# Kernel tuning notes

Measured on AMD Instinct MI355X. Metric: run time of the kernel, lower is better.

## Reference

```python
import jax, jax.numpy as jnp
import numpy as np

LOG_PROB_FACTOR = 0.5  # logProbFactor


def setup_inputs() -> dict:
    key = jax.random.key(0)
    ks = jax.random.split(key, 8)
    B, L, F, K = 2048, 512, 64, 2
    s = jax.random.randint(ks[0], (B, L), 0, K)
    W0 = jax.random.normal(ks[1], (K, F), jnp.float32) / np.sqrt(K).astype(np.float32)
    b0 = jnp.zeros((F,), jnp.float32)
    # fused LSTM weights, gate order (i, f, g, o); flax: dense_i no bias, dense_h has bias
    Wi = jax.random.normal(ks[2], (F, 4 * F), jnp.float32) / np.sqrt(F).astype(np.float32)
    Wh = jax.random.normal(ks[3], (F, 4 * F), jnp.float32) / np.sqrt(F).astype(np.float32)
    bh = jnp.zeros((4 * F,), jnp.float32)
    Wa = jax.random.normal(ks[4], (F, K), jnp.float32) / np.sqrt(F).astype(np.float32)
    ba = jnp.zeros((K,), jnp.float32)
    Wp = jax.random.normal(ks[5], (F, 1), jnp.float32) / np.sqrt(F).astype(np.float32)
    bp = jnp.zeros((1,), jnp.float32)
    return {"s": s, "W0": W0, "b0": b0, "Wi": Wi, "Wh": Wh, "bh": bh,
            "Wa": Wa, "ba": ba, "Wp": Wp, "bp": bp}


def _forward(s, W0, b0, Wi, Wh, bh, Wa, ba, Wp, bp):
    B, L = s.shape
    K, F = W0.shape
    # pad a leading zero token: input at step t is spin at site t-1
    s_pad = jnp.pad(s, ((0, 0), (1, 0)))                       # [B, L+1]
    x = jax.nn.one_hot(s_pad, K, dtype=W0.dtype) @ W0 + b0     # layer0: [B, L+1, F]
    xs = jnp.swapaxes(x, 0, 1)                                 # [L+1, B, F] time-major
    c0 = jnp.zeros((B, F), x.dtype)
    h0 = jnp.zeros((B, F), x.dtype)

    def step(carry, xt):
        c, h = carry
        g = xt @ Wi + h @ Wh + bh                              # [B, 4F]
        i, f, gg, o = jnp.split(g, 4, axis=-1)
        cn = jax.nn.sigmoid(f) * c + jax.nn.sigmoid(i) * jnp.tanh(gg)
        hn = jax.nn.sigmoid(o) * jnp.tanh(cn)
        return (cn, hn), hn

    _, ys = jax.lax.scan(step, (c0, h0), xs)                   # [L+1, B, F]

    logits = ys[:-1] @ Wa + ba                                 # [L, B, K]
    logp = jax.nn.log_softmax(logits, axis=-1) * LOG_PROB_FACTOR
    picked = jnp.take_along_axis(logp, s.T[..., None], axis=-1)[..., 0]  # [L, B]
    amp = picked.sum(axis=0)                                   # [B]
    phase = (ys[-1] @ Wp + bp)[..., 0]                         # [B]
    return amp + 1j * phase                                    # complex log-psi per sample


def reference(s, W0, b0, Wi, Wh, bh, Wa, ba, Wp, bp):
    return _forward(s, W0, b0, Wi, Wh, bh, Wa, ba, Wp, bp)
```

## Files before the change

kernel.cpp:

```cpp
#include <hip/hip_runtime.h>
#include <math.h>

typedef _Float16 f16x8 __attribute__((ext_vector_type(8)));
typedef float    f32x4 __attribute__((ext_vector_type(4)));
typedef _Float16 f16x2 __attribute__((ext_vector_type(2)));
typedef __fp16   fp16x2 __attribute__((ext_vector_type(2)));

#define B_TOT 2048
#define LSEQ  512
#define NS    4
#define LOG2E 1.44269504088896f
#define LN2   0.69314718055995f

#define MFMA16(A, B, C) __builtin_amdgcn_mfma_f32_16x16x32_f16((A), (B), (C), 0, 0, 0)

__global__ __launch_bounds__(256, 2)
void lstm_v18_kernel(const int* __restrict__ s,
                     const float* __restrict__ W0, const float* __restrict__ b0,
                     const float* __restrict__ Wi, const float* __restrict__ Wh,
                     const float* __restrict__ bh, const float* __restrict__ Wa,
                     const float* __restrict__ ba, const float* __restrict__ Wp,
                     const float* __restrict__ bp, float* __restrict__ out)
{
    const int tid  = threadIdx.x;
    const int w    = tid >> 6;
    const int lane = tid & 63;
    const int n    = lane & 15;
    const int q    = lane >> 4;
    const int ns   = n & 3;
    const int cp   = n >> 2;
    const int b0s  = blockIdx.x * NS;

    __shared__ __align__(16) unsigned int HhD[2][128];
    __shared__ unsigned char  TOKW[LSEQ + 2];
    __shared__ unsigned char  SRAW[NS][LSEQ];
    __shared__ _Float16 DBUF[LSEQ][NS];
    __shared__ float PART[64][NS];

    for (int i = tid; i < NS * LSEQ; i += 256)
        SRAW[i >> 9][i & 511] = (unsigned char)s[(b0s + (i >> 9)) * LSEQ + (i & 511)];
    __syncthreads();
    for (int u = tid; u <= LSEQ; u += 256) {
        unsigned int mask = 0;
        if (u >= 1) {
            #pragma unroll
            for (int m = 0; m < NS; ++m)
                mask |= ((unsigned int)SRAW[m][u - 1]) << m;
        }
        TOKW[u] = (unsigned char)mask;
    }

    f16x8 awh[4][2];
    #pragma unroll
    for (int g = 0; g < 4; ++g) {
        const float sc  = (g == 2) ? (2.0f * LOG2E) : (-LOG2E);
        const int   col = 64 * g + 16 * w + n;
        #pragma unroll
        for (int c = 0; c < 2; ++c)
            #pragma unroll
            for (int j = 0; j < 8; ++j)
                awh[g][c][j] = (_Float16)(Wh[(32 * c + 8 * q + j) * 256 + col] * sc);
    }

    f16x8 awd[2];
    #pragma unroll
    for (int c = 0; c < 2; ++c)
        #pragma unroll
        for (int j = 0; j < 8; ++j) {
            int k = 32 * c + 8 * q + j;
            awd[c][j] = (_Float16)((n == 0) ? (Wa[2 * k + 1] - Wa[2 * k]) : 0.0f);
        }
    const float dba = ba[1] - ba[0];

    f32x4 p0q[4], dpq[4];
    {
        float a0[4][4], a1[4][4];
        #pragma unroll
        for (int g = 0; g < 4; ++g)
            #pragma unroll
            for (int r = 0; r < 4; ++r) {
                float bb = bh[64 * g + 16 * w + 4 * q + r];
                a0[g][r] = bb; a1[g][r] = bb;
            }
        for (int f = 0; f < 64; ++f) {
            float wb0 = W0[f]      + b0[f];
            float wb1 = W0[64 + f] + b0[f];
            #pragma unroll
            for (int g = 0; g < 4; ++g) {
                const float4 wi4 = *(const float4*)&Wi[f * 256 + 64 * g + 16 * w + 4 * q];
                #pragma unroll
                for (int r = 0; r < 4; ++r) {
                    float wi = (&wi4.x)[r];
                    a0[g][r] = fmaf(wb0, wi, a0[g][r]);
                    a1[g][r] = fmaf(wb1, wi, a1[g][r]);
                }
            }
        }
        #pragma unroll
        for (int g = 0; g < 4; ++g) {
            const float sc = (g == 2) ? (2.0f * LOG2E) : (-LOG2E);
            #pragma unroll
            for (int r = 0; r < 4; ++r) {
                p0q[g][r] = a0[g][r] * sc;
                dpq[g][r] = (a1[g][r] - a0[g][r]) * sc;
            }
        }
    }

    __syncthreads();

    const int wIdx = 64 * ns + 16 * w + 4 * q + cp;
    const int rAddr = 32 * ns + 4 * q;

    float h1 = 0.f, c1 = 0.f;
    f32x4 ci[4];
    #pragma unroll
    for (int g = 0; g < 4; ++g) ci[g] = p0q[g];

    float dpend = 0.0f;
    int   tpend = -1;

    #pragma unroll 4
    for (int v = 0; v <= LSEQ; ++v) {
        const int p = v & 1;
        unsigned int* __restrict__ hb = &HhD[p][0];

        ((_Float16*)hb)[wIdx] = (_Float16)h1;
        __syncthreads();

        if (tpend >= 0) {
            if (lane < NS) DBUF[tpend][lane] = (_Float16)dpend;
            tpend = -1;
        }

        uint4 r0 = *(const uint4*)&hb[rAddr];
        uint4 r1 = *(const uint4*)&hb[rAddr + 16];
        const f16x8 bf0 = __builtin_bit_cast(f16x8, r0);
        const f16x8 bf1 = __builtin_bit_cast(f16x8, r1);

        const unsigned int tokm_next = (v < LSEQ) ? (unsigned int)TOKW[v + 1] : 0u;

        f32x4 acc0 = ci[0], acc1 = ci[1], acc2 = ci[2], acc3 = ci[3];
        acc0 = MFMA16(awh[0][0], bf0, acc0);
        acc1 = MFMA16(awh[1][0], bf0, acc1);
        acc2 = MFMA16(awh[2][0], bf0, acc2);
        acc3 = MFMA16(awh[3][0], bf0, acc3);
        acc0 = MFMA16(awh[0][1], bf1, acc0);
        acc1 = MFMA16(awh[1][1], bf1, acc1);
        acc2 = MFMA16(awh[2][1], bf1, acc2);
        acc3 = MFMA16(awh[3][1], bf1, acc3);

        if (v >= 1 && w == (v & 3)) {
            f32x4 da = (f32x4){dba, dba, dba, dba};
            da = MFMA16(awd[0], bf0, da);
            da = MFMA16(awd[1], bf1, da);
            dpend = da[0];
            tpend = v - 1;
        }

        const float sel = (float)((tokm_next >> ns) & 1u);
        const f32x4 sel4 = {sel, sel, sel, sel};
        #pragma unroll
        for (int g = 0; g < 4; ++g)
            ci[g] = dpq[g] * sel4 + p0q[g];

        const bool s1 = (cp & 1) != 0;
        const bool s2 = (cp & 2) != 0;
        float gi = s2 ? (s1 ? acc0[3] : acc0[2]) : (s1 ? acc0[1] : acc0[0]);
        float gf = s2 ? (s1 ? acc1[3] : acc1[2]) : (s1 ? acc1[1] : acc1[0]);
        float gg = s2 ? (s1 ? acc2[3] : acc2[2]) : (s1 ? acc2[1] : acc2[0]);
        float go = s2 ? (s1 ? acc3[3] : acc3[2]) : (s1 ? acc3[1] : acc3[0]);

        {
            float ei = __builtin_amdgcn_exp2f(gi);
            float ef = __builtin_amdgcn_exp2f(gf);
            float eg = __builtin_amdgcn_exp2f(gg);
            float eo = __builtin_amdgcn_exp2f(go);
            float P  = (1.0f + ei) * (eg + 1.0f);
            float F  = 1.0f + ef;
            float R2 = __builtin_amdgcn_rcpf(P * F);
            float cn = fmaf(c1 * P, R2, (eg - 1.0f) * F * R2);
            c1 = cn;
            float ec = __builtin_amdgcn_exp2f(fminf(cn * (2.0f * LOG2E), 60.f));
            float Ro = __builtin_amdgcn_rcpf((1.0f + eo) * (ec + 1.0f));
            h1 = (ec - 1.0f) * Ro;
        }
    }

    if (tpend >= 0 && lane < NS) DBUF[tpend][lane] = (_Float16)dpend;
    ((_Float16*)&HhD[1][0])[wIdx] = (_Float16)h1;
    __syncthreads();

    {
        const int nn = tid & 3;
        const int cc = tid >> 2;
        float a = 0.0f;
        #pragma unroll 4
        for (int k = 0; k < 8; ++k) {
            int t = cc * 8 + k;
            float d = (float)DBUF[t][nn];
            float x = SRAW[nn][t] ? -d : d;
            float e = __builtin_amdgcn_exp2f(-fabsf(x) * LOG2E);
            a += fmaxf(x, 0.0f) + __builtin_amdgcn_logf(1.0f + e) * LN2;
        }
        PART[cc][nn] = a;
    }
    __syncthreads();

    if (tid < NS) {
        float ssum = 0.0f;
        #pragma unroll
        for (int c = 0; c < 64; ++c) ssum += PART[c][tid];
        out[b0s + tid] = -0.5f * ssum;
    }

    if (w == 0) {
        unsigned int ua = HhD[1][32 * q + 2 * n];
        unsigned int ub = HhD[1][32 * q + 2 * n + 1];
        f16x2 ha = __builtin_bit_cast(f16x2, ua);
        f16x2 hc = __builtin_bit_cast(f16x2, ub);
        float ph = fmaf((float)ha[0], Wp[4 * n],
                   fmaf((float)ha[1], Wp[4 * n + 1],
                   fmaf((float)hc[0], Wp[4 * n + 2],
                        (float)hc[1] * Wp[4 * n + 3])));
        ph += __shfl_xor(ph, 1, 64);
        ph += __shfl_xor(ph, 2, 64);
        ph += __shfl_xor(ph, 4, 64);
        ph += __shfl_xor(ph, 8, 64);
        if (n == 0) out[B_TOT + b0s + q] = ph + bp[0];
    }
}

extern "C" void kernel_launch(void* const* d_in, const int* in_sizes, int n_in,
                              void* d_out, int out_size, void* d_ws, size_t ws_size,
                              hipStream_t stream) {
    const int*   s  = (const int*)  d_in[0];
    const float* W0 = (const float*)d_in[1];
    const float* b0 = (const float*)d_in[2];
    const float* Wi = (const float*)d_in[3];
    const float* Wh = (const float*)d_in[4];
    const float* bh = (const float*)d_in[5];
    const float* Wa = (const float*)d_in[6];
    const float* ba = (const float*)d_in[7];
    const float* Wp = (const float*)d_in[8];
    const float* bp = (const float*)d_in[9];
    float* out = (float*)d_out;

    dim3 grid(B_TOT / NS);
    dim3 block(256);
    lstm_v18_kernel<<<grid, block, 0, stream>>>(s, W0, b0, Wi, Wh, bh,
                                                Wa, ba, Wp, bp, out);
}
```

Measured before the change: 303.7 us.

## Halve LSTM block to two waves, each computing eight gate tiles per step

```diff
diff --git a/kernel.cpp b/kernel.cpp
--- a/kernel.cpp
+++ b/kernel.cpp
@@ -3,7 +3,6 @@
 
 typedef _Float16 f16x8 __attribute__((ext_vector_type(8)));
 typedef float    f32x4 __attribute__((ext_vector_type(4)));
-typedef _Float16 f16x2 __attribute__((ext_vector_type(2)));
 typedef __fp16   fp16x2 __attribute__((ext_vector_type(2)));
 
 #define B_TOT 2048
@@ -14,8 +13,13 @@
 
 #define MFMA16(A, B, C) __builtin_amdgcn_mfma_f32_16x16x32_f16((A), (B), (C), 0, 0, 0)
 
-__global__ __launch_bounds__(256, 2)
-void lstm_v18_kernel(const int* __restrict__ s,
+__device__ __forceinline__ unsigned int pkrtz(float a, float b) {
+    fp16x2 p = __builtin_amdgcn_cvt_pkrtz(a, b);
+    return __builtin_bit_cast(unsigned int, p);
+}
+
+__global__ __launch_bounds__(128, 1)
+void lstm_v19_kernel(const int* __restrict__ s,
                      const float* __restrict__ W0, const float* __restrict__ b0,
                      const float* __restrict__ Wi, const float* __restrict__ Wh,
                      const float* __restrict__ bh, const float* __restrict__ Wa,
@@ -23,24 +27,27 @@
                      const float* __restrict__ bp, float* __restrict__ out)
 {
     const int tid  = threadIdx.x;
-    const int w    = tid >> 6;
+    const int w2   = tid >> 6;
     const int lane = tid & 63;
     const int n    = lane & 15;
     const int q    = lane >> 4;
     const int ns   = n & 3;
     const int cp   = n >> 2;
+    const int hp   = cp >> 1;
+    const int pp   = cp & 1;
     const int b0s  = blockIdx.x * NS;
 
     __shared__ __align__(16) unsigned int HhD[2][128];
     __shared__ unsigned char  TOKW[LSEQ + 2];
     __shared__ unsigned char  SRAW[NS][LSEQ];
     __shared__ _Float16 DBUF[LSEQ][NS];
-    __shared__ float PART[64][NS];
-
-    for (int i = tid; i < NS * LSEQ; i += 256)
+    __shared__ float PART[32][NS];
+    __shared__ float PHS[2][NS];
+
+    for (int i = tid; i < NS * LSEQ; i += 128)
         SRAW[i >> 9][i & 511] = (unsigned char)s[(b0s + (i >> 9)) * LSEQ + (i & 511)];
     __syncthreads();
-    for (int u = tid; u <= LSEQ; u += 256) {
+    for (int u = tid; u <= LSEQ; u += 128) {
         unsigned int mask = 0;
         if (u >= 1) {
             #pragma unroll
@@ -50,16 +57,17 @@
         TOKW[u] = (unsigned char)mask;
     }
 
-    f16x8 awh[4][2];
+    f16x8 awh[8][2];
     #pragma unroll
-    for (int g = 0; g < 4; ++g) {
-        const float sc  = (g == 2) ? (2.0f * LOG2E) : (-LOG2E);
-        const int   col = 64 * g + 16 * w + n;
+    for (int t = 0; t < 8; ++t) {
+        const int   gt  = t >> 1;
+        const float sc  = (gt == 2) ? (2.0f * LOG2E) : (-LOG2E);
+        const int   col = 64 * gt + 32 * w2 + 16 * (t & 1) + n;
         #pragma unroll
         for (int c = 0; c < 2; ++c)
             #pragma unroll
             for (int j = 0; j < 8; ++j)
-                awh[g][c][j] = (_Float16)(Wh[(32 * c + 8 * q + j) * 256 + col] * sc);
+                awh[t][c][j] = (_Float16)(Wh[(32 * c + 8 * q + j) * 256 + col] * sc);
     }
 
     f16x8 awd[2];
@@ -72,60 +80,61 @@
         }
     const float dba = ba[1] - ba[0];
 
-    f32x4 p0q[4], dpq[4];
+    f32x4 p0q[8], dpq[8];
     {
-        float a0[4][4], a1[4][4];
-        #pragma unroll
-        for (int g = 0; g < 4; ++g)
+        f32x4 A0[8], A1[8];
+        #pragma unroll
+        for (int t = 0; t < 8; ++t)
             #pragma unroll
             for (int r = 0; r < 4; ++r) {
-                float bb = bh[64 * g + 16 * w + 4 * q + r];
-                a0[g][r] = bb; a1[g][r] = bb;
+                float bb = bh[64 * (t >> 1) + 32 * w2 + 16 * (t & 1) + 4 * q + r];
+                A0[t][r] = bb; A1[t][r] = bb;
             }
         for (int f = 0; f < 64; ++f) {
             float wb0 = W0[f]      + b0[f];
             float wb1 = W0[64 + f] + b0[f];
             #pragma unroll
-            for (int g = 0; g < 4; ++g) {
-                const float4 wi4 = *(const float4*)&Wi[f * 256 + 64 * g + 16 * w + 4 * q];
+            for (int t = 0; t < 8; ++t) {
+                const float4 wi4 = *(const float4*)
+                    &Wi[f * 256 + 64 * (t >> 1) + 32 * w2 + 16 * (t & 1) + 4 * q];
                 #pragma unroll
                 for (int r = 0; r < 4; ++r) {
-                    float wi = (&wi4.x)[r];
-                    a0[g][r] = fmaf(wb0, wi, a0[g][r]);
-                    a1[g][r] = fmaf(wb1, wi, a1[g][r]);
+                    float wv = (&wi4.x)[r];
+                    A0[t][r] = fmaf(wb0, wv, A0[t][r]);
+                    A1[t][r] = fmaf(wb1, wv, A1[t][r]);
                 }
             }
         }
         #pragma unroll
-        for (int g = 0; g < 4; ++g) {
-            const float sc = (g == 2) ? (2.0f * LOG2E) : (-LOG2E);
+        for (int t = 0; t < 8; ++t) {
+            const float sc = ((t >> 1) == 2) ? (2.0f * LOG2E) : (-LOG2E);
             #pragma unroll
             for (int r = 0; r < 4; ++r) {
-                p0q[g][r] = a0[g][r] * sc;
-                dpq[g][r] = (a1[g][r] - a0[g][r]) * sc;
+                p0q[t][r] = A0[t][r] * sc;
+                dpq[t][r] = (A1[t][r] - A0[t][r]) * sc;
             }
         }
     }
 
     __syncthreads();
 
-    const int wIdx = 64 * ns + 16 * w + 4 * q + cp;
-    const int rAddr = 32 * ns + 4 * q;
-
-    float h1 = 0.f, c1 = 0.f;
-    f32x4 ci[4];
+    const int wAddr = 64 * w2 + 32 * hp + 16 * (q >> 1) + 4 * ns + 2 * (q & 1) + pp;
+    const int rAddr = 16 * q + 4 * ns;
+
+    float h2[2] = {0.f, 0.f}, c2[2] = {0.f, 0.f};
+    f32x4 ci[8];
     #pragma unroll
-    for (int g = 0; g < 4; ++g) ci[g] = p0q[g];
+    for (int t = 0; t < 8; ++t) ci[t] = p0q[t];
 
     float dpend = 0.0f;
     int   tpend = -1;
 
-    #pragma unroll 4
+    #pragma unroll 2
     for (int v = 0; v <= LSEQ; ++v) {
         const int p = v & 1;
         unsigned int* __restrict__ hb = &HhD[p][0];
 
-        ((_Float16*)hb)[wIdx] = (_Float16)h1;
+        hb[wAddr] = pkrtz(h2[0], h2[1]);
         __syncthreads();
 
         if (tpend >= 0) {
@@ -134,23 +143,19 @@
         }
 
         uint4 r0 = *(const uint4*)&hb[rAddr];
-        uint4 r1 = *(const uint4*)&hb[rAddr + 16];
+        uint4 r1 = *(const uint4*)&hb[rAddr + 64];
         const f16x8 bf0 = __builtin_bit_cast(f16x8, r0);
         const f16x8 bf1 = __builtin_bit_cast(f16x8, r1);
 
         const unsigned int tokm_next = (v < LSEQ) ? (unsigned int)TOKW[v + 1] : 0u;
 
-        f32x4 acc0 = ci[0], acc1 = ci[1], acc2 = ci[2], acc3 = ci[3];
-        acc0 = MFMA16(awh[0][0], bf0, acc0);
-        acc1 = MFMA16(awh[1][0], bf0, acc1);
-        acc2 = MFMA16(awh[2][0], bf0, acc2);
-        acc3 = MFMA16(awh[3][0], bf0, acc3);
-        acc0 = MFMA16(awh[0][1], bf1, acc0);
-        acc1 = MFMA16(awh[1][1], bf1, acc1);
-        acc2 = MFMA16(awh[2][1], bf1, acc2);
-        acc3 = MFMA16(awh[3][1], bf1, acc3);
-
-        if (v >= 1 && w == (v & 3)) {
+        f32x4 acc[8];
+        #pragma unroll
+        for (int t = 0; t < 8; ++t) acc[t] = MFMA16(awh[t][0], bf0, ci[t]);
+        #pragma unroll
+        for (int t = 0; t < 8; ++t) acc[t] = MFMA16(awh[t][1], bf1, acc[t]);
+
+        if (v >= 1 && w2 == (v & 1)) {
             f32x4 da = (f32x4){dba, dba, dba, dba};
             da = MFMA16(awd[0], bf0, da);
             da = MFMA16(awd[1], bf1, da);
@@ -161,34 +166,55 @@
         const float sel = (float)((tokm_next >> ns) & 1u);
         const f32x4 sel4 = {sel, sel, sel, sel};
         #pragma unroll
-        for (int g = 0; g < 4; ++g)
-            ci[g] = dpq[g] * sel4 + p0q[g];
-
-        const bool s1 = (cp & 1) != 0;
-        const bool s2 = (cp & 2) != 0;
-        float gi = s2 ? (s1 ? acc0[3] : acc0[2]) : (s1 ? acc0[1] : acc0[0]);
-        float gf = s2 ? (s1 ? acc1[3] : acc1[2]) : (s1 ? acc1[1] : acc1[0]);
-        float gg = s2 ? (s1 ? acc2[3] : acc2[2]) : (s1 ? acc2[1] : acc2[0]);
-        float go = s2 ? (s1 ? acc3[3] : acc3[2]) : (s1 ? acc3[1] : acc3[0]);
-
-        {
-            float ei = __builtin_amdgcn_exp2f(gi);
-            float ef = __builtin_amdgcn_exp2f(gf);
-            float eg = __builtin_amdgcn_exp2f(gg);
-            float eo = __builtin_amdgcn_exp2f(go);
+        for (int t = 0; t < 8; ++t)
+            ci[t] = dpq[t] * sel4 + p0q[t];
+
+        const bool pb = (pp != 0);
+        const bool hbv = (hp != 0);
+        float g0[2], g1[2], g2[2], g3[2];
+        #pragma unroll
+        for (int gt = 0; gt < 4; ++gt) {
+            const f32x4 ta = acc[2 * gt];
+            const f32x4 tb = acc[2 * gt + 1];
+            float z0 = pb ? ta[2] : ta[0];
+            float z1 = pb ? ta[3] : ta[1];
+            float z2 = pb ? tb[2] : tb[0];
+            float z3 = pb ? tb[3] : tb[1];
+            float x0 = hbv ? z2 : z0;
+            float x1 = hbv ? z3 : z1;
+            if (gt == 0) { g0[0] = x0; g0[1] = x1; }
+            if (gt == 1) { g1[0] = x0; g1[1] = x1; }
+            if (gt == 2) { g2[0] = x0; g2[1] = x1; }
+            if (gt == 3) { g3[0] = x0; g3[1] = x1; }
+        }
+
+        #pragma unroll
+        for (int jj = 0; jj < 2; ++jj) {
+            float ei = __builtin_amdgcn_exp2f(g0[jj]);
+            float ef = __builtin_amdgcn_exp2f(g1[jj]);
+            float eg = __builtin_amdgcn_exp2f(g2[jj]);
+            float eo = __builtin_amdgcn_exp2f(g3[jj]);
             float P  = (1.0f + ei) * (eg + 1.0f);
             float F  = 1.0f + ef;
             float R2 = __builtin_amdgcn_rcpf(P * F);
-            float cn = fmaf(c1 * P, R2, (eg - 1.0f) * F * R2);
-            c1 = cn;
+            float cn = fmaf(c2[jj] * P, R2, (eg - 1.0f) * F * R2);
+            c2[jj] = cn;
             float ec = __builtin_amdgcn_exp2f(fminf(cn * (2.0f * LOG2E), 60.f));
             float Ro = __builtin_amdgcn_rcpf((1.0f + eo) * (ec + 1.0f));
-            h1 = (ec - 1.0f) * Ro;
+            h2[jj] = (ec - 1.0f) * Ro;
         }
     }
 
     if (tpend >= 0 && lane < NS) DBUF[tpend][lane] = (_Float16)dpend;
-    ((_Float16*)&HhD[1][0])[wIdx] = (_Float16)h1;
+    {
+        const int f = 32 * w2 + 16 * hp + 4 * q + 2 * pp;
+        float ph = fmaf(h2[0], Wp[f], h2[1] * Wp[f + 1]);
+        ph += __shfl_xor(ph, 4, 64);
+        ph += __shfl_xor(ph, 8, 64);
+        ph += __shfl_xor(ph, 16, 64);
+        ph += __shfl_xor(ph, 32, 64);
+        if (lane < NS) PHS[w2][lane] = ph;
+    }
     __syncthreads();
 
     {
@@ -196,8 +222,8 @@
         const int cc = tid >> 2;
         float a = 0.0f;
         #pragma unroll 4
-        for (int k = 0; k < 8; ++k) {
-            int t = cc * 8 + k;
+        for (int k = 0; k < 16; ++k) {
+            int t = cc * 16 + k;
             float d = (float)DBUF[t][nn];
             float x = SRAW[nn][t] ? -d : d;
             float e = __builtin_amdgcn_exp2f(-fabsf(x) * LOG2E);
@@ -210,24 +236,9 @@
     if (tid < NS) {
         float ssum = 0.0f;
         #pragma unroll
-        for (int c = 0; c < 64; ++c) ssum += PART[c][tid];
+        for (int c = 0; c < 32; ++c) ssum += PART[c][tid];
         out[b0s + tid] = -0.5f * ssum;
-    }
-
-    if (w == 0) {
-        unsigned int ua = HhD[1][32 * q + 2 * n];
-        unsigned int ub = HhD[1][32 * q + 2 * n + 1];
-        f16x2 ha = __builtin_bit_cast(f16x2, ua);
-        f16x2 hc = __builtin_bit_cast(f16x2, ub);
-        float ph = fmaf((float)ha[0], Wp[4 * n],
-                   fmaf((float)ha[1], Wp[4 * n + 1],
-                   fmaf((float)hc[0], Wp[4 * n + 2],
-                        (float)hc[1] * Wp[4 * n + 3])));
-        ph += __shfl_xor(ph, 1, 64);
-        ph += __shfl_xor(ph, 2, 64);
-        ph += __shfl_xor(ph, 4, 64);
-        ph += __shfl_xor(ph, 8, 64);
-        if (n == 0) out[B_TOT + b0s + q] = ph + bp[0];
+        out[B_TOT + b0s + tid] = PHS[0][tid] + PHS[1][tid] + bp[0];
     }
 }
 
@@ -247,7 +258,7 @@
     float* out = (float*)d_out;
 
     dim3 grid(B_TOT / NS);
-    dim3 block(256);
-    lstm_v18_kernel<<<grid, block, 0, stream>>>(s, W0, b0, Wi, Wh, bh,
+    dim3 block(128);
+    lstm_v19_kernel<<<grid, block, 0, stream>>>(s, W0, b0, Wi, Wh, bh,
                                                 Wa, ba, Wp, bp, out);
 }
```

Result: slower. 432.5 us (+42.4%).

## Process two independent 4-sample chains per block to interleave MFMA and barrier latency

Applied to the files above, without the earlier changes.

```diff
diff --git a/kernel.cpp b/kernel.cpp
--- a/kernel.cpp
+++ b/kernel.cpp
@@ -3,19 +3,18 @@
 
 typedef _Float16 f16x8 __attribute__((ext_vector_type(8)));
 typedef float    f32x4 __attribute__((ext_vector_type(4)));
-typedef _Float16 f16x2 __attribute__((ext_vector_type(2)));
 typedef __fp16   fp16x2 __attribute__((ext_vector_type(2)));
 
 #define B_TOT 2048
 #define LSEQ  512
-#define NS    4
+#define NSC   4
 #define LOG2E 1.44269504088896f
 #define LN2   0.69314718055995f
 
 #define MFMA16(A, B, C) __builtin_amdgcn_mfma_f32_16x16x32_f16((A), (B), (C), 0, 0, 0)
 
-__global__ __launch_bounds__(256, 2)
-void lstm_v18_kernel(const int* __restrict__ s,
+__global__ __launch_bounds__(256, 1)
+void lstm_v20_kernel(const int* __restrict__ s,
                      const float* __restrict__ W0, const float* __restrict__ b0,
                      const float* __restrict__ Wi, const float* __restrict__ Wh,
                      const float* __restrict__ bh, const float* __restrict__ Wa,
@@ -29,22 +28,23 @@
     const int q    = lane >> 4;
     const int ns   = n & 3;
     const int cp   = n >> 2;
-    const int b0s  = blockIdx.x * NS;
-
-    __shared__ __align__(16) unsigned int HhD[2][128];
+    const int b0s  = blockIdx.x * 8;
+
+    __shared__ __align__(16) unsigned int HhX[2][2][128];
     __shared__ unsigned char  TOKW[LSEQ + 2];
-    __shared__ unsigned char  SRAW[NS][LSEQ];
-    __shared__ _Float16 DBUF[LSEQ][NS];
-    __shared__ float PART[64][NS];
-
-    for (int i = tid; i < NS * LSEQ; i += 256)
+    __shared__ unsigned char  SRAW[8][LSEQ];
+    __shared__ _Float16 DBUF[LSEQ][8];
+    __shared__ float PART[32][8];
+    __shared__ float PHS[4][2][NSC];
+
+    for (int i = tid; i < 8 * LSEQ; i += 256)
         SRAW[i >> 9][i & 511] = (unsigned char)s[(b0s + (i >> 9)) * LSEQ + (i & 511)];
     __syncthreads();
     for (int u = tid; u <= LSEQ; u += 256) {
         unsigned int mask = 0;
         if (u >= 1) {
             #pragma unroll
-            for (int m = 0; m < NS; ++m)
+            for (int m = 0; m < 8; ++m)
                 mask |= ((unsigned int)SRAW[m][u - 1]) << m;
         }
         TOKW[u] = (unsigned char)mask;
@@ -109,69 +109,95 @@
 
     __syncthreads();
 
-    const int wIdx = 64 * ns + 16 * w + 4 * q + cp;
-    const int rAddr = 32 * ns + 4 * q;
-
-    float h1 = 0.f, c1 = 0.f;
-    f32x4 ci[4];
+    const int m4    = 4 * q + cp;
+    const int bsel  = m4 >> 3;
+    const int jj16  = m4 & 7;
+    const int chunk = 2 * w + bsel;
+    const int baseD = 8 * ns + 4 * (chunk & 1) + 32 * ((chunk >> 1) & 1)
+                    + 64 * (chunk >> 2);
+    const int wIdx  = 2 * baseD + jj16;
+    const int rA    = 8 * ns + 4 * (q & 1) + 32 * (q >> 1);
+
+    float hA = 0.f, cA = 0.f, hB = 0.f, cB = 0.f;
+    f32x4 ciA[4], ciB[4];
     #pragma unroll
-    for (int g = 0; g < 4; ++g) ci[g] = p0q[g];
-
-    float dpend = 0.0f;
-    int   tpend = -1;
+    for (int g = 0; g < 4; ++g) { ciA[g] = p0q[g]; ciB[g] = p0q[g]; }
+
+    float dpA = 0.f, dpB = 0.f;
+    int   tpA = -1,  tpB = -1;
 
     #pragma unroll 4
     for (int v = 0; v <= LSEQ; ++v) {
         const int p = v & 1;
-        unsigned int* __restrict__ hb = &HhD[p][0];
-
-        ((_Float16*)hb)[wIdx] = (_Float16)h1;
+        _Float16* __restrict__ h16A = (_Float16*)&HhX[p][0][0];
+        _Float16* __restrict__ h16B = (_Float16*)&HhX[p][1][0];
+
+        h16A[wIdx] = (_Float16)hA;
+        h16B[wIdx] = (_Float16)hB;
         __syncthreads();
 
-        if (tpend >= 0) {
-            if (lane < NS) DBUF[tpend][lane] = (_Float16)dpend;
-            tpend = -1;
-        }
-
-        uint4 r0 = *(const uint4*)&hb[rAddr];
-        uint4 r1 = *(const uint4*)&hb[rAddr + 16];
-        const f16x8 bf0 = __builtin_bit_cast(f16x8, r0);
-        const f16x8 bf1 = __builtin_bit_cast(f16x8, r1);
-
-        const unsigned int tokm_next = (v < LSEQ) ? (unsigned int)TOKW[v + 1] : 0u;
-
-        f32x4 acc0 = ci[0], acc1 = ci[1], acc2 = ci[2], acc3 = ci[3];
-        acc0 = MFMA16(awh[0][0], bf0, acc0);
-        acc1 = MFMA16(awh[1][0], bf0, acc1);
-        acc2 = MFMA16(awh[2][0], bf0, acc2);
-        acc3 = MFMA16(awh[3][0], bf0, acc3);
-        acc0 = MFMA16(awh[0][1], bf1, acc0);
-        acc1 = MFMA16(awh[1][1], bf1, acc1);
-        acc2 = MFMA16(awh[2][1], bf1, acc2);
-        acc3 = MFMA16(awh[3][1], bf1, acc3);
+        const uint4 ra0 = *(const uint4*)&HhX[p][0][rA];
+        const uint4 ra1 = *(const uint4*)&HhX[p][0][rA + 64];
+        const uint4 rb0 = *(const uint4*)&HhX[p][1][rA];
+        const uint4 rb1 = *(const uint4*)&HhX[p][1][rA + 64];
+        const f16x8 bfA0 = __builtin_bit_cast(f16x8, ra0);
+        const f16x8 bfA1 = __builtin_bit_cast(f16x8, ra1);
+        const f16x8 bfB0 = __builtin_bit_cast(f16x8, rb0);
+        const f16x8 bfB1 = __builtin_bit_cast(f16x8, rb1);
+
+        if (tpA >= 0) { if (lane < NSC) DBUF[tpA][lane] = (_Float16)dpA; tpA = -1; }
+        if (tpB >= 0) { if (lane < NSC) DBUF[tpB][4 + lane] = (_Float16)dpB; tpB = -1; }
+
+        const unsigned int tok = (v < LSEQ) ? (unsigned int)TOKW[v + 1] : 0u;
+
+        f32x4 aA0 = ciA[0], aA1 = ciA[1], aA2 = ciA[2], aA3 = ciA[3];
+        f32x4 aB0 = ciB[0], aB1 = ciB[1], aB2 = ciB[2], aB3 = ciB[3];
+        aA0 = MFMA16(awh[0][0], bfA0, aA0);  aB0 = MFMA16(awh[0][0], bfB0, aB0);
+        aA1 = MFMA16(awh[1][0], bfA0, aA1);  aB1 = MFMA16(awh[1][0], bfB0, aB1);
+        aA2 = MFMA16(awh[2][0], bfA0, aA2);  aB2 = MFMA16(awh[2][0], bfB0, aB2);
+        aA3 = MFMA16(awh[3][0], bfA0, aA3);  aB3 = MFMA16(awh[3][0], bfB0, aB3);
+        aA0 = MFMA16(awh[0][1], bfA1, aA0);  aB0 = MFMA16(awh[0][1], bfB1, aB0);
+        aA1 = MFMA16(awh[1][1], bfA1, aA1);  aB1 = MFMA16(awh[1][1], bfB1, aB1);
+        aA2 = MFMA16(awh[2][1], bfA1, aA2);  aB2 = MFMA16(awh[2][1], bfB1, aB2);
+        aA3 = MFMA16(awh[3][1], bfA1, aA3);  aB3 = MFMA16(awh[3][1], bfB1, aB3);
 
         if (v >= 1 && w == (v & 3)) {
             f32x4 da = (f32x4){dba, dba, dba, dba};
-            da = MFMA16(awd[0], bf0, da);
-            da = MFMA16(awd[1], bf1, da);
-            dpend = da[0];
-            tpend = v - 1;
-        }
-
-        const float sel = (float)((tokm_next >> ns) & 1u);
-        const f32x4 sel4 = {sel, sel, sel, sel};
-        #pragma unroll
-        for (int g = 0; g < 4; ++g)
-            ci[g] = dpq[g] * sel4 + p0q[g];
+            da = MFMA16(awd[0], bfA0, da);
+            da = MFMA16(awd[1], bfA1, da);
+            dpA = da[0];
+            tpA = v - 1;
+        }
+        if (v >= 1 && w == ((v + 2) & 3)) {
+            f32x4 db = (f32x4){dba, dba, dba, dba};
+            db = MFMA16(awd[0], bfB0, db);
+            db = MFMA16(awd[1], bfB1, db);
+            dpB = db[0];
+            tpB = v - 1;
+        }
+
+        const float sA = (float)((tok >> ns) & 1u);
+        const float sB = (float)((tok >> (4 + ns)) & 1u);
+        const f32x4 sA4 = {sA, sA, sA, sA};
+        const f32x4 sB4 = {sB, sB, sB, sB};
+        #pragma unroll
+        for (int g = 0; g < 4; ++g) {
+            ciA[g] = dpq[g] * sA4 + p0q[g];
+            ciB[g] = dpq[g] * sB4 + p0q[g];
+        }
 
         const bool s1 = (cp & 1) != 0;
         const bool s2 = (cp & 2) != 0;
-        float gi = s2 ? (s1 ? acc0[3] : acc0[2]) : (s1 ? acc0[1] : acc0[0]);
-        float gf = s2 ? (s1 ? acc1[3] : acc1[2]) : (s1 ? acc1[1] : acc1[0]);
-        float gg = s2 ? (s1 ? acc2[3] : acc2[2]) : (s1 ? acc2[1] : acc2[0]);
-        float go = s2 ? (s1 ? acc3[3] : acc3[2]) : (s1 ? acc3[1] : acc3[0]);
-
-        {
+        #pragma unroll
+        for (int cc = 0; cc < 2; ++cc) {
+            const f32x4 x0 = cc ? aB0 : aA0;
+            const f32x4 x1 = cc ? aB1 : aA1;
+            const f32x4 x2 = cc ? aB2 : aA2;
+            const f32x4 x3 = cc ? aB3 : aA3;
+            float gi = s2 ? (s1 ? x0[3] : x0[2]) : (s1 ? x0[1] : x0[0]);
+            float gf = s2 ? (s1 ? x1[3] : x1[2]) : (s1 ? x1[1] : x1[0]);
+            float gg = s2 ? (s1 ? x2[3] : x2[2]) : (s1 ? x2[1] : x2[0]);
+            float go = s2 ? (s1 ? x3[3] : x3[2]) : (s1 ? x3[1] : x3[0]);
             float ei = __builtin_amdgcn_exp2f(gi);
             float ef = __builtin_amdgcn_exp2f(gf);
             float eg = __builtin_amdgcn_exp2f(gg);
@@ -179,25 +205,37 @@
             float P  = (1.0f + ei) * (eg + 1.0f);
             float F  = 1.0f + ef;
             float R2 = __builtin_amdgcn_rcpf(P * F);
-            float cn = fmaf(c1 * P, R2, (eg - 1.0f) * F * R2);
-            c1 = cn;
+            float cold = cc ? cB : cA;
+            float cn = fmaf(cold * P, R2, (eg - 1.0f) * F * R2);
             float ec = __builtin_amdgcn_exp2f(fminf(cn * (2.0f * LOG2E), 60.f));
             float Ro = __builtin_amdgcn_rcpf((1.0f + eo) * (ec + 1.0f));
-            h1 = (ec - 1.0f) * Ro;
-        }
-    }
-
-    if (tpend >= 0 && lane < NS) DBUF[tpend][lane] = (_Float16)dpend;
-    ((_Float16*)&HhD[1][0])[wIdx] = (_Float16)h1;
-    __syncthreads();
+            float hn = (ec - 1.0f) * Ro;
+            if (cc) { cB = cn; hB = hn; } else { cA = cn; hA = hn; }
+        }
+    }
+
+    if (tpA >= 0 && lane < NSC) DBUF[tpA][lane] = (_Float16)dpA;
+    if (tpB >= 0 && lane < NSC) DBUF[tpB][4 + lane] = (_Float16)dpB;
 
     {
-        const int nn = tid & 3;
-        const int cc = tid >> 2;
+        const int f = 16 * w + 4 * q + cp;
+        float phA = hA * Wp[f];
+        float phB = hB * Wp[f];
+        phA += __shfl_xor(phA, 4, 64);  phB += __shfl_xor(phB, 4, 64);
+        phA += __shfl_xor(phA, 8, 64);  phB += __shfl_xor(phB, 8, 64);
+        phA += __shfl_xor(phA, 16, 64); phB += __shfl_xor(phB, 16, 64);
+        phA += __shfl_xor(phA, 32, 64); phB += __shfl_xor(phB, 32, 64);
+        if (lane < NSC) { PHS[w][0][lane] = phA; PHS[w][1][lane] = phB; }
+    }
+    __syncthreads();
+
+    {
+        const int nn = tid & 7;
+        const int cc = tid >> 3;
         float a = 0.0f;
         #pragma unroll 4
-        for (int k = 0; k < 8; ++k) {
-            int t = cc * 8 + k;
+        for (int k = 0; k < 16; ++k) {
+            int t = cc * 16 + k;
             float d = (float)DBUF[t][nn];
             float x = SRAW[nn][t] ? -d : d;
             float e = __builtin_amdgcn_exp2f(-fabsf(x) * LOG2E);
@@ -207,27 +245,14 @@
     }
     __syncthreads();
 
-    if (tid < NS) {
+    if (tid < 8) {
         float ssum = 0.0f;
         #pragma unroll
-        for (int c = 0; c < 64; ++c) ssum += PART[c][tid];
+        for (int c = 0; c < 32; ++c) ssum += PART[c][tid];
         out[b0s + tid] = -0.5f * ssum;
-    }
-
-    if (w == 0) {
-        unsigned int ua = HhD[1][32 * q + 2 * n];
-        unsigned int ub = HhD[1][32 * q + 2 * n + 1];
-        f16x2 ha = __builtin_bit_cast(f16x2, ua);
-        f16x2 hc = __builtin_bit_cast(f16x2, ub);
-        float ph = fmaf((float)ha[0], Wp[4 * n],
-                   fmaf((float)ha[1], Wp[4 * n + 1],
-                   fmaf((float)hc[0], Wp[4 * n + 2],
-                        (float)hc[1] * Wp[4 * n + 3])));
-        ph += __shfl_xor(ph, 1, 64);
-        ph += __shfl_xor(ph, 2, 64);
-        ph += __shfl_xor(ph, 4, 64);
-        ph += __shfl_xor(ph, 8, 64);
-        if (n == 0) out[B_TOT + b0s + q] = ph + bp[0];
+        float ph = PHS[0][tid >> 2][tid & 3] + PHS[1][tid >> 2][tid & 3]
+                 + PHS[2][tid >> 2][tid & 3] + PHS[3][tid >> 2][tid & 3];
+        out[B_TOT + b0s + tid] = ph + bp[0];
     }
 }
 
@@ -246,8 +271,8 @@
     const float* bp = (const float*)d_in[9];
     float* out = (float*)d_out;
 
-    dim3 grid(B_TOT / NS);
+    dim3 grid(B_TOT / 8);
     dim3 block(256);
-    lstm_v18_kernel<<<grid, block, 0, stream>>>(s, W0, b0, Wi, Wh, bh,
+    lstm_v20_kernel<<<grid, block, 0, stream>>>(s, W0, b0, Wi, Wh, bh,
                                                 Wa, ba, Wp, bp, out);
 }
```

Result: slower. 397.1 us (+30.8%).

## Process one sample per single-wave block, removing per-step block barriers

Applied to the files above, without the earlier changes.

```diff
diff --git a/kernel.cpp b/kernel.cpp
--- a/kernel.cpp
+++ b/kernel.cpp
@@ -3,65 +3,70 @@
 
 typedef _Float16 f16x8 __attribute__((ext_vector_type(8)));
 typedef float    f32x4 __attribute__((ext_vector_type(4)));
-typedef _Float16 f16x2 __attribute__((ext_vector_type(2)));
-typedef __fp16   fp16x2 __attribute__((ext_vector_type(2)));
 
 #define B_TOT 2048
 #define LSEQ  512
-#define NS    4
 #define LOG2E 1.44269504088896f
 #define LN2   0.69314718055995f
 
 #define MFMA16(A, B, C) __builtin_amdgcn_mfma_f32_16x16x32_f16((A), (B), (C), 0, 0, 0)
 
-__global__ __launch_bounds__(256, 2)
-void lstm_v18_kernel(const int* __restrict__ s,
+__global__ __launch_bounds__(64, 2)
+void lstm_v21_kernel(const int* __restrict__ s,
                      const float* __restrict__ W0, const float* __restrict__ b0,
                      const float* __restrict__ Wi, const float* __restrict__ Wh,
                      const float* __restrict__ bh, const float* __restrict__ Wa,
                      const float* __restrict__ ba, const float* __restrict__ Wp,
                      const float* __restrict__ bp, float* __restrict__ out)
 {
-    const int tid  = threadIdx.x;
-    const int w    = tid >> 6;
-    const int lane = tid & 63;
+    const int lane = threadIdx.x;
     const int n    = lane & 15;
     const int q    = lane >> 4;
-    const int ns   = n & 3;
-    const int cp   = n >> 2;
-    const int b0s  = blockIdx.x * NS;
+    const int slot = n & 3;
+    const int cT   = n >> 2;
+    const int b    = blockIdx.x;
+    const int fo   = 4 * q + slot + 16 * cT;
 
-    __shared__ __align__(16) unsigned int HhD[2][128];
-    __shared__ unsigned char  TOKW[LSEQ + 2];
-    __shared__ unsigned char  SRAW[NS][LSEQ];
-    __shared__ _Float16 DBUF[LSEQ][NS];
-    __shared__ float PART[64][NS];
+    __shared__ __align__(16) _Float16 HX[64];
+    __shared__ _Float16 DB[LSEQ];
+    __shared__ unsigned char TOK[LSEQ + 4];
 
-    for (int i = tid; i < NS * LSEQ; i += 256)
-        SRAW[i >> 9][i & 511] = (unsigned char)s[(b0s + (i >> 9)) * LSEQ + (i & 511)];
-    __syncthreads();
-    for (int u = tid; u <= LSEQ; u += 256) {
-        unsigned int mask = 0;
-        if (u >= 1) {
-            #pragma unroll
-            for (int m = 0; m < NS; ++m)
-                mask |= ((unsigned int)SRAW[m][u - 1]) << m;
+    #pragma unroll
+    for (int j = 0; j < 8; ++j) {
+        int t = lane + 64 * j;
+        TOK[t + 1] = (unsigned char)s[b * LSEQ + t];
+    }
+    if (lane == 0) { TOK[0] = 0; TOK[LSEQ + 1] = 0; TOK[LSEQ + 2] = 0; }
+
+    float p0v[4], p1v[4];
+    #pragma unroll
+    for (int g = 0; g < 4; ++g) { float bb = bh[64 * g + fo]; p0v[g] = bb; p1v[g] = bb; }
+    for (int k = 0; k < 64; ++k) {
+        float wb0 = W0[k]      + b0[k];
+        float wb1 = W0[64 + k] + b0[k];
+        #pragma unroll
+        for (int g = 0; g < 4; ++g) {
+            float wi = Wi[k * 256 + 64 * g + fo];
+            p0v[g] = fmaf(wb0, wi, p0v[g]);
+            p1v[g] = fmaf(wb1, wi, p1v[g]);
         }
-        TOKW[u] = (unsigned char)mask;
+    }
+    #pragma unroll
+    for (int g = 0; g < 4; ++g) {
+        const float sc = (g == 2) ? (2.0f * LOG2E) : (-LOG2E);
+        p0v[g] *= sc; p1v[g] *= sc;
     }
 
-    f16x8 awh[4][2];
+    f16x8 awh[16][2];
     #pragma unroll
-    for (int g = 0; g < 4; ++g) {
-        const float sc  = (g == 2) ? (2.0f * LOG2E) : (-LOG2E);
-        const int   col = 64 * g + 16 * w + n;
+    for (int t = 0; t < 16; ++t) {
+        const float sc = ((t >> 2) == 2) ? (2.0f * LOG2E) : (-LOG2E);
         #pragma unroll
         for (int c = 0; c < 2; ++c)
             #pragma unroll
             for (int j = 0; j < 8; ++j)
-                awh[g][c][j] = (_Float16)(Wh[(32 * c + 8 * q + j) * 256 + col] * sc);
+                awh[t][c][j] = (_Float16)(Wh[(32 * c + 8 * q + j) * 256 + 16 * t + n] * sc);
     }
-
     f16x8 awd[2];
     #pragma unroll
     for (int c = 0; c < 2; ++c)
@@ -72,110 +77,55 @@
         }
     const float dba = ba[1] - ba[0];
 
-    f32x4 p0q[4], dpq[4];
-    {
-        float a0[4][4], a1[4][4];
-        #pragma unroll
-        for (int g = 0; g < 4; ++g)
-            #pragma unroll
-            for (int r = 0; r < 4; ++r) {
-                float bb = bh[64 * g + 16 * w + 4 * q + r];
-                a0[g][r] = bb; a1[g][r] = bb;
-            }
-        for (int f = 0; f < 64; ++f) {
-            float wb0 = W0[f]      + b0[f];
-            float wb1 = W0[64 + f] + b0[f];
-            #pragma unroll
-            for (int g = 0; g < 4; ++g) {
-                const float4 wi4 = *(const float4*)&Wi[f * 256 + 64 * g + 16 * w + 4 * q];
-                #pragma unroll
-                for (int r = 0; r < 4; ++r) {
-                    float wi = (&wi4.x)[r];
-                    a0[g][r] = fmaf(wb0, wi, a0[g][r]);
-                    a1[g][r] = fmaf(wb1, wi, a1[g][r]);
-                }
-            }
+    __syncthreads();
+
+    const bool is0 = (slot == 0), is1 = (slot == 1), is2 = (slot == 2), is3 = (slot == 3);
+    const bool t1 = (cT == 1), t2 = (cT == 2), t3 = (cT == 3);
+
+    float h1 = 0.f, c1 = 0.f;
+    int tokc = 0;
+
+    for (int v = 0; v <= LSEQ; ++v) {
+        HX[fo] = (_Float16)h1;
+        const f16x8 bf0 = *(const f16x8*)&HX[8 * q];
+        const f16x8 bf1 = *(const f16x8*)&HX[32 + 8 * q];
+        const int tokn = TOK[v + 1];
+
+        if (v >= 1) {
+            f32x4 dv = {dba, dba, dba, dba};
+            dv = MFMA16(awd[0], bf0, dv);
+            dv = MFMA16(awd[1], bf1, dv);
+            if (lane == 0) DB[v - 1] = (_Float16)dv[0];
         }
+
+        float gv[4];
         #pragma unroll
         for (int g = 0; g < 4; ++g) {
-            const float sc = (g == 2) ? (2.0f * LOG2E) : (-LOG2E);
-            #pragma unroll
-            for (int r = 0; r < 4; ++r) {
-                p0q[g][r] = a0[g][r] * sc;
-                dpq[g][r] = (a1[g][r] - a0[g][r]) * sc;
-            }
+            const float pv = tokc ? p1v[g] : p0v[g];
+            const f32x4 Cv = { is0 ? pv : 0.f, is1 ? pv : 0.f,
+                               is2 ? pv : 0.f, is3 ? pv : 0.f };
+            f32x4 m0 = MFMA16(awh[4 * g + 0][0], bf0, Cv);
+            f32x4 m1 = MFMA16(awh[4 * g + 1][0], bf0, Cv);
+            f32x4 m2 = MFMA16(awh[4 * g + 2][0], bf0, Cv);
+            f32x4 m3 = MFMA16(awh[4 * g + 3][0], bf0, Cv);
+            m0 = MFMA16(awh[4 * g + 0][1], bf1, m0);
+            m1 = MFMA16(awh[4 * g + 1][1], bf1, m1);
+            m2 = MFMA16(awh[4 * g + 2][1], bf1, m2);
+            m3 = MFMA16(awh[4 * g + 3][1], bf1, m3);
+            float s0 = m0[0]; s0 = is1 ? m0[1] : s0; s0 = is2 ? m0[2] : s0; s0 = is3 ? m0[3] : s0;
+            float s1 = m1[0]; s1 = is1 ? m1[1] : s1; s1 = is2 ? m1[2] : s1; s1 = is3 ? m1[3] : s1;
+            float s2 = m2[0]; s2 = is1 ? m2[1] : s2; s2 = is2 ? m2[2] : s2; s2 = is3 ? m2[3] : s2;
+            float s3 = m3[0]; s3 = is1 ? m3[1] : s3; s3 = is2 ? m3[2] : s3; s3 = is3 ? m3[3] : s3;
+            float x = s0; x = t1 ? s1 : x; x = t2 ? s2 : x; x = t3 ? s3 : x;
+            gv[g] = x;
         }
-    }
-
-    __syncthreads();
-
-    const int wIdx = 64 * ns + 16 * w + 4 * q + cp;
-    const int rAddr = 32 * ns + 4 * q;
-
-    float h1 = 0.f, c1 = 0.f;
-    f32x4 ci[4];
-    #pragma unroll
-    for (int g = 0; g < 4; ++g) ci[g] = p0q[g];
-
-    float dpend = 0.0f;
-    int   tpend = -1;
-
-    #pragma unroll 4
-    for (int v = 0; v <= LSEQ; ++v) {
-        const int p = v & 1;
-        unsigned int* __restrict__ hb = &HhD[p][0];
-
-        ((_Float16*)hb)[wIdx] = (_Float16)h1;
-        __syncthreads();
-
-        if (tpend >= 0) {
-            if (lane < NS) DBUF[tpend][lane] = (_Float16)dpend;
-            tpend = -1;
-        }
-
-        uint4 r0 = *(const uint4*)&hb[rAddr];
-        uint4 r1 = *(const uint4*)&hb[rAddr + 16];
-        const f16x8 bf0 = __builtin_bit_cast(f16x8, r0);
-        const f16x8 bf1 = __builtin_bit_cast(f16x8, r1);
-
-        const unsigned int tokm_next = (v < LSEQ) ? (unsigned int)TOKW[v + 1] : 0u;
-
-        f32x4 acc0 = ci[0], acc1 = ci[1], acc2 = ci[2], acc3 = ci[3];
-        acc0 = MFMA16(awh[0][0], bf0, acc0);
-        acc1 = MFMA16(awh[1][0], bf0, acc1);
-        acc2 = MFMA16(awh[2][0], bf0, acc2);
-        acc3 = MFMA16(awh[3][0], bf0, acc3);
-        acc0 = MFMA16(awh[0][1], bf1, acc0);
-        acc1 = MFMA16(awh[1][1], bf1, acc1);
-        acc2 = MFMA16(awh[2][1], bf1, acc2);
-        acc3 = MFMA16(awh[3][1], bf1, acc3);
-
-        if (v >= 1 && w == (v & 3)) {
-            f32x4 da = (f32x4){dba, dba, dba, dba};
-            da = MFMA16(awd[0], bf0, da);
-            da = MFMA16(awd[1], bf1, da);
-            dpend = da[0];
-            tpend = v - 1;
-        }
-
-        const float sel = (float)((tokm_next >> ns) & 1u);
-        const f32x4 sel4 = {sel, sel, sel, sel};
-        #pragma unroll
-        for (int g = 0; g < 4; ++g)
-            ci[g] = dpq[g] * sel4 + p0q[g];
-
-        const bool s1 = (cp & 1) != 0;
-        const bool s2 = (cp & 2) != 0;
-        float gi = s2 ? (s1 ? acc0[3] : acc0[2]) : (s1 ? acc0[1] : acc0[0]);
-        float gf = s2 ? (s1 ? acc1[3] : acc1[2]) : (s1 ? acc1[1] : acc1[0]);
-        float gg = s2 ? (s1 ? acc2[3] : acc2[2]) : (s1 ? acc2[1] : acc2[0]);
-        float go = s2 ? (s1 ? acc3[3] : acc3[2]) : (s1 ? acc3[1] : acc3[0]);
+        tokc = tokn;
 
         {
-            float ei = __builtin_amdgcn_exp2f(gi);
-            float ef = __builtin_amdgcn_exp2f(gf);
-            float eg = __builtin_amdgcn_exp2f(gg);
-            float eo = __builtin_amdgcn_exp2f(go);
+            float ei = __builtin_amdgcn_exp2f(gv[0]);
+            float ef = __builtin_amdgcn_exp2f(gv[1]);
+            float eg = __builtin_amdgcn_exp2f(gv[2]);
+            float eo = __builtin_amdgcn_exp2f(gv[3]);
             float P  = (1.0f + ei) * (eg + 1.0f);
             float F  = 1.0f + ef;
             float R2 = __builtin_amdgcn_rcpf(P * F);
@@ -187,47 +137,26 @@
         }
     }
 
-    if (tpend >= 0 && lane < NS) DBUF[tpend][lane] = (_Float16)dpend;
-    ((_Float16*)&HhD[1][0])[wIdx] = (_Float16)h1;
     __syncthreads();
 
-    {
-        const int nn = tid & 3;
-        const int cc = tid >> 2;
-        float a = 0.0f;
-        #pragma unroll 4
-        for (int k = 0; k < 8; ++k) {
-            int t = cc * 8 + k;
-            float d = (float)DBUF[t][nn];
-            float x = SRAW[nn][t] ? -d : d;
-            float e = __builtin_amdgcn_exp2f(-fabsf(x) * LOG2E);
-            a += fmaxf(x, 0.0f) + __builtin_amdgcn_logf(1.0f + e) * LN2;
-        }
-        PART[cc][nn] = a;
+    float aa = 0.f;
+    #pragma unroll 2
+    for (int j = 0; j < 8; ++j) {
+        int t = lane + 64 * j;
+        float d = (float)DB[t];
+        float x = TOK[t + 1] ? -d : d;
+        float e = __builtin_amdgcn_exp2f(-fabsf(x) * LOG2E);
+        aa += fmaxf(x, 0.f) + __builtin_amdgcn_logf(1.0f + e) * LN2;
     }
-    __syncthreads();
-
-    if (tid < NS) {
-        float ssum = 0.0f;
-        #pragma unroll
-        for (int c = 0; c < 64; ++c) ssum += PART[c][tid];
-        out[b0s + tid] = -0.5f * ssum;
+    float ph = h1 * Wp[fo];
+    #pragma unroll
+    for (int m = 1; m < 64; m <<= 1) {
+        aa += __shfl_xor(aa, m, 64);
+        ph += __shfl_xor(ph, m, 64);
     }
-
-    if (w == 0) {
-        unsigned int ua = HhD[1][32 * q + 2 * n];
-        unsigned int ub = HhD[1][32 * q + 2 * n + 1];
-        f16x2 ha = __builtin_bit_cast(f16x2, ua);
-        f16x2 hc = __builtin_bit_cast(f16x2, ub);
-        float ph = fmaf((float)ha[0], Wp[4 * n],
-                   fmaf((float)ha[1], Wp[4 * n + 1],
-                   fmaf((float)hc[0], Wp[4 * n + 2],
-                        (float)hc[1] * Wp[4 * n + 3])));
-        ph += __shfl_xor(ph, 1, 64);
-        ph += __shfl_xor(ph, 2, 64);
-        ph += __shfl_xor(ph, 4, 64);
-        ph += __shfl_xor(ph, 8, 64);
-        if (n == 0) out[B_TOT + b0s + q] = ph + bp[0];
+    if (lane == 0) {
+        out[b]         = -0.5f * aa;
+        out[B_TOT + b] = ph + bp[0];
     }
 }
 
@@ -246,8 +175,8 @@
     const float* bp = (const float*)d_in[9];
     float* out = (float*)d_out;
 
-    dim3 grid(B_TOT / NS);
-    dim3 block(256);
-    lstm_v18_kernel<<<grid, block, 0, stream>>>(s, W0, b0, Wi, Wh, bh,
+    dim3 grid(B_TOT);
+    dim3 block(64);
+    lstm_v21_kernel<<<grid, block, 0, stream>>>(s, W0, b0, Wi, Wh, bh,
                                                 Wa, ba, Wp, bp, out);
 }
```

Measured after the change: 544.4 us. 1.79x slower.
